# Optimization experiments

Hardware: AMD Instinct MI355X
Metric: run time of the kernel (lower is better)

## Reference

```python
import jax, jax.numpy as jnp
import numpy as np

N_NODES = 50000
N_EDGES = 400000
DIMS = [512, 512, 512, 512]  # input + 3 hidden
NUM_CLASSES = 40


def setup_inputs() -> dict:
    key = jax.random.key(0)
    ks = jax.random.split(key, 16)
    feat = jax.random.normal(ks[0], (N_NODES, DIMS[0]), dtype=jnp.float32)
    src = jax.random.randint(ks[1], (N_EDGES,), 0, N_NODES, dtype=jnp.int32)
    dst = jax.random.randint(ks[2], (N_EDGES,), 0, N_NODES, dtype=jnp.int32)
    params = {}
    for i in range(3):
        fan_in = DIMS[i]
        s = 1.0 / np.sqrt(fan_in)
        params[f"W{i}"] = jax.random.uniform(ks[3 + 2 * i], (DIMS[i], DIMS[i + 1]), jnp.float32, -s, s)
        params[f"b{i}"] = jax.random.uniform(ks[4 + 2 * i], (DIMS[i + 1],), jnp.float32, -s, s)
    s = 1.0 / np.sqrt(DIMS[-1])
    params["Wc"] = jax.random.uniform(ks[10], (DIMS[-1], NUM_CLASSES), jnp.float32, -s, s)
    params["bc"] = jax.random.uniform(ks[11], (NUM_CLASSES,), jnp.float32, -s, s)
    return {"feat": feat, "src": src, "dst": dst, **params}


def _gin_layer(h, src, dst, W, b):
    # DGL GINConv, aggregator='sum', eps=0: rst = (1+eps)*h + sum_{j in N(i)} h_j
    agg = jax.ops.segment_sum(h[src], dst, num_segments=N_NODES)  # [N, D]
    return jax.nn.relu((h + agg) @ W + b)  # apply_func Linear, then relu (dropout p=0)


def reference(feat, src, dst, W0, b0, W1, b1, W2, b2, Wc, bc):
    h = _gin_layer(feat, src, dst, W0, b0)
    h = _gin_layer(h, src, dst, W1, b1)
    h = _gin_layer(h, src, dst, W2, b2)
    return h @ Wc + bc  # [N, num_classes]
```

## Files before the change

kernel.cpp:

```cpp
#include <hip/hip_runtime.h>

#define N_NODES 50000
#define N_EDGES 400000
#define D 512
#define NCLS 40
#define SCAN_BLOCKS ((N_NODES + 255) / 256)

typedef __attribute__((ext_vector_type(8))) __bf16 bf16x8;
typedef __attribute__((ext_vector_type(4))) float f32x4;
typedef __attribute__((ext_vector_type(4))) float float4v;
typedef __attribute__((ext_vector_type(8))) unsigned short ushort8v;
typedef __attribute__((ext_vector_type(4))) unsigned short ushort4v;

__device__ __forceinline__ float bf2f(unsigned short u) {
  union { unsigned int i; float f; } v; v.i = ((unsigned int)u) << 16; return v.f;
}
__device__ __forceinline__ unsigned short f2bf(float f) {
  union { float f; unsigned int i; } v; v.f = f;
  unsigned int u = v.i;
  u += 0x7fffu + ((u >> 16) & 1u);
  return (unsigned short)(u >> 16);
}

__global__ void hist_kernel(const int* __restrict__ dst, int* __restrict__ counts) {
  int e = blockIdx.x * blockDim.x + threadIdx.x;
  if (e < N_EDGES) atomicAdd(&counts[dst[e]], 1);
}

__global__ __launch_bounds__(256) void scan_local_kernel(const int* __restrict__ counts,
    int* __restrict__ incl, int* __restrict__ bsum) {
  __shared__ int s[256];
  int i = blockIdx.x * 256 + threadIdx.x;
  int v = (i < N_NODES) ? counts[i] : 0;
  s[threadIdx.x] = v;
  __syncthreads();
#pragma unroll
  for (int o = 1; o < 256; o <<= 1) {
    int t = (threadIdx.x >= o) ? s[threadIdx.x - o] : 0;
    __syncthreads();
    s[threadIdx.x] += t;
    __syncthreads();
  }
  if (i < N_NODES) incl[i] = s[threadIdx.x];
  if (threadIdx.x == 255) bsum[blockIdx.x] = s[255];
}

__global__ __launch_bounds__(256) void scan_bsum_kernel(int* __restrict__ bsum) {
  __shared__ int s[256];
  int v = (threadIdx.x < SCAN_BLOCKS) ? bsum[threadIdx.x] : 0;
  s[threadIdx.x] = v;
  __syncthreads();
#pragma unroll
  for (int o = 1; o < 256; o <<= 1) {
    int t = (threadIdx.x >= o) ? s[threadIdx.x - o] : 0;
    __syncthreads();
    s[threadIdx.x] += t;
    __syncthreads();
  }
  if (threadIdx.x < SCAN_BLOCKS) bsum[threadIdx.x] = s[threadIdx.x] - v;
}

__global__ __launch_bounds__(256) void scan_finish_kernel(const int* __restrict__ counts,
    const int* __restrict__ bsum, int* __restrict__ row_ptr, int* __restrict__ cursor) {
  int i = blockIdx.x * 256 + threadIdx.x;
  if (i < N_NODES) {
    int inc = cursor[i] + bsum[blockIdx.x];
    row_ptr[i + 1] = inc;
    cursor[i] = inc - counts[i];
    if (i == 0) row_ptr[0] = 0;
  }
}

__global__ void fill_kernel(const int* __restrict__ src, const int* __restrict__ dst,
                            int* __restrict__ cursor, int* __restrict__ esrc) {
  int e = blockIdx.x * blockDim.x + threadIdx.x;
  if (e < N_EDGES) {
    int pos = atomicAdd(&cursor[dst[e]], 1);
    esrc[pos] = src[e];
  }
}

__global__ void cvt_feat_kernel(const float* __restrict__ feat, unsigned short* __restrict__ hb) {
  size_t i = (size_t)(blockIdx.x * blockDim.x + threadIdx.x) * 4;
  if (i < (size_t)N_NODES * D) {
    float4v v = *(const float4v*)&feat[i];
    ushort4v o;
    o[0] = f2bf(v[0]); o[1] = f2bf(v[1]); o[2] = f2bf(v[2]); o[3] = f2bf(v[3]);
    *(ushort4v*)&hb[i] = o;
  }
}

__global__ void cvt_w_kernel(const float* __restrict__ W, unsigned short* __restrict__ Wt) {
  int i = blockIdx.x * blockDim.x + threadIdx.x;
  int n = i >> 9, k = i & 511;
  Wt[i] = f2bf(W[k * D + n]);
}

__global__ void cvt_wc_kernel(const float* __restrict__ Wc, unsigned short* __restrict__ Wct) {
  int i = blockIdx.x * blockDim.x + threadIdx.x;
  if (i < 48 * D) {
    int n = i >> 9, k = i & 511;
    Wct[i] = (n < NCLS) ? f2bf(Wc[k * NCLS + n]) : (unsigned short)0;
  }
}

__global__ __launch_bounds__(256) void agg_kernel(const unsigned short* __restrict__ hb,
    const int* __restrict__ row_ptr, const int* __restrict__ esrc,
    unsigned short* __restrict__ zb) {
  int w = threadIdx.x >> 6, lane = threadIdx.x & 63;
  int node = blockIdx.x * 4 + w;
  int col = lane * 8;
  const unsigned short* hcol = hb + col;
  float acc[8];
  ushort8v v = *(const ushort8v*)&hcol[(size_t)node * D];
#pragma unroll
  for (int t = 0; t < 8; ++t) acc[t] = bf2f(v[t]);
  int s = row_ptr[node], e = row_ptr[node + 1];
  int j = s;
  for (; j + 4 <= e; j += 4) {
    int i0 = esrc[j + 0];
    int i1 = esrc[j + 1];
    int i2 = esrc[j + 2];
    int i3 = esrc[j + 3];
    ushort8v v0 = *(const ushort8v*)&hcol[(size_t)i0 * D];
    ushort8v v1 = *(const ushort8v*)&hcol[(size_t)i1 * D];
    ushort8v v2 = *(const ushort8v*)&hcol[(size_t)i2 * D];
    ushort8v v3 = *(const ushort8v*)&hcol[(size_t)i3 * D];
#pragma unroll
    for (int t = 0; t < 8; ++t) acc[t] += bf2f(v0[t]);
#pragma unroll
    for (int t = 0; t < 8; ++t) acc[t] += bf2f(v1[t]);
#pragma unroll
    for (int t = 0; t < 8; ++t) acc[t] += bf2f(v2[t]);
#pragma unroll
    for (int t = 0; t < 8; ++t) acc[t] += bf2f(v3[t]);
  }
  for (; j < e; ++j) {
    int sn = esrc[j];
    ushort8v nv = *(const ushort8v*)&hcol[(size_t)sn * D];
#pragma unroll
    for (int t = 0; t < 8; ++t) acc[t] += bf2f(nv[t]);
  }
  ushort8v o;
#pragma unroll
  for (int t = 0; t < 8; ++t) o[t] = f2bf(acc[t]);
  *(ushort8v*)&zb[(size_t)node * D + col] = o;
}

__global__ __launch_bounds__(256) void gemm_kernel(
    const unsigned short* __restrict__ Z, const unsigned short* __restrict__ Wt,
    const float* __restrict__ bias, unsigned short* __restrict__ Hout, int M) {
  __shared__ unsigned short smem[128 * 132];
  unsigned short* As = smem;
  unsigned short* Bs = smem + 4096;
  const int n0 = blockIdx.x * 128;
  const int m0 = blockIdx.y * 128;
  const int tid = threadIdx.x;
  const int lane = tid & 63;
  const int w = tid >> 6;
  const int wm = (w & 1) * 64;
  const int wn = (w >> 1) * 64;
  const int quad = lane >> 4;
  const int r16 = lane & 15;

  f32x4 acc[4][4];
#pragma unroll
  for (int i = 0; i < 4; ++i)
#pragma unroll
    for (int j = 0; j < 4; ++j)
      acc[i][j] = (f32x4){0.f, 0.f, 0.f, 0.f};

  const int c0 = w * 2;
  for (int kt = 0; kt < 16; ++kt) {
    __syncthreads();
    const int kbase = kt * 32;
#pragma unroll
    for (int c = 0; c < 2; ++c) {
      int chunk = c0 + c;
      int mrow = chunk * 16 + (lane >> 2);
      int kk = kbase + (lane & 3) * 8;
      int gm = m0 + mrow; if (gm > M - 1) gm = M - 1;
      __builtin_amdgcn_global_load_lds(
          (__attribute__((address_space(1))) void*)(void*)(Z + (size_t)gm * D + kk),
          (__attribute__((address_space(3))) void*)(As + chunk * 512),
          16, 0, 0);
      int nrow = n0 + mrow;
      __builtin_amdgcn_global_load_lds(
          (__attribute__((address_space(1))) void*)(void*)(Wt + (size_t)nrow * D + kk),
          (__attribute__((address_space(3))) void*)(Bs + chunk * 512),
          16, 0, 0);
    }
    __syncthreads();

    bf16x8 a[4], b[4];
#pragma unroll
    for (int i = 0; i < 4; ++i) {
      a[i] = *(const bf16x8*)&As[(wm + i * 16 + r16) * 32 + quad * 8];
      b[i] = *(const bf16x8*)&Bs[(wn + i * 16 + r16) * 32 + quad * 8];
    }
#pragma unroll
    for (int i = 0; i < 4; ++i)
#pragma unroll
      for (int j = 0; j < 4; ++j)
        acc[i][j] = __builtin_amdgcn_mfma_f32_16x16x32_bf16(a[i], b[j], acc[i][j], 0, 0, 0);
  }

  __syncthreads();
  unsigned short* Cs = smem;
#pragma unroll
  for (int j = 0; j < 4; ++j) {
    float bv = bias[n0 + wn + j * 16 + r16];
#pragma unroll
    for (int i = 0; i < 4; ++i) {
      int crow = wm + i * 16 + quad * 4;
      int ccol = wn + j * 16 + r16;
#pragma unroll
      for (int r = 0; r < 4; ++r) {
        float vv = acc[i][j][r] + bv;
        vv = vv > 0.f ? vv : 0.f;
        Cs[(crow + r) * 132 + ccol] = f2bf(vv);
      }
    }
  }
  __syncthreads();
#pragma unroll
  for (int it = 0; it < 8; ++it) {
    int row = w * 32 + it * 4 + (lane >> 4);
    int colofs = (lane & 15) * 8;
    int gm = m0 + row;
    if (gm < M) {
      ushort8v vv = *(const ushort8v*)&Cs[row * 132 + colofs];
      *(ushort8v*)&Hout[(size_t)gm * D + n0 + colofs] = vv;
    }
  }
}

__global__ __launch_bounds__(256) void cls_kernel(const unsigned short* __restrict__ hb,
    const unsigned short* __restrict__ Wct, const float* __restrict__ bc,
    float* __restrict__ out) {
  int w = threadIdx.x >> 6, lane = threadIdx.x & 63;
  int quad = lane >> 4, r16 = lane & 15;
  int nb = blockIdx.x * 64 + w * 16;
  int arow = nb + r16; if (arow > N_NODES - 1) arow = N_NODES - 1;
  f32x4 acc[3];
#pragma unroll
  for (int j = 0; j < 3; ++j) acc[j] = (f32x4){0.f, 0.f, 0.f, 0.f};
#pragma unroll 4
  for (int kt = 0; kt < 16; ++kt) {
    int kk = kt * 32 + quad * 8;
    bf16x8 a = *(const bf16x8*)&hb[(size_t)arow * D + kk];
#pragma unroll
    for (int j = 0; j < 3; ++j) {
      bf16x8 b = *(const bf16x8*)&Wct[(size_t)(j * 16 + r16) * D + kk];
      acc[j] = __builtin_amdgcn_mfma_f32_16x16x32_bf16(a, b, acc[j], 0, 0, 0);
    }
  }
#pragma unroll
  for (int j = 0; j < 3; ++j) {
    int gn = j * 16 + r16;
    if (gn < NCLS) {
      float bv = bc[gn];
#pragma unroll
      for (int r = 0; r < 4; ++r) {
        int gm = nb + quad * 4 + r;
        if (gm < N_NODES) out[(size_t)gm * NCLS + gn] = acc[j][r] + bv;
      }
    }
  }
}

extern "C" void kernel_launch(void* const* d_in, const int* in_sizes, int n_in,
                              void* d_out, int out_size, void* d_ws, size_t ws_size,
                              hipStream_t stream) {
  const float* feat = (const float*)d_in[0];
  const int* src = (const int*)d_in[1];
  const int* dst = (const int*)d_in[2];
  const float* W0 = (const float*)d_in[3];
  const float* b0 = (const float*)d_in[4];
  const float* W1 = (const float*)d_in[5];
  const float* b1 = (const float*)d_in[6];
  const float* W2 = (const float*)d_in[7];
  const float* b2 = (const float*)d_in[8];
  const float* Wc = (const float*)d_in[9];
  const float* bc = (const float*)d_in[10];
  float* out = (float*)d_out;

  char* ws = (char*)d_ws;
  size_t off = 0;
  auto alloc = [&](size_t bytes) {
    char* p = ws + off;
    off += (bytes + 255) & ~(size_t)255;
    return p;
  };
  unsigned short* hb = (unsigned short*)alloc((size_t)N_NODES * D * 2);
  unsigned short* zb = (unsigned short*)alloc((size_t)N_NODES * D * 2);
  unsigned short* Wt = (unsigned short*)alloc((size_t)3 * D * D * 2);
  unsigned short* Wct = (unsigned short*)alloc((size_t)48 * D * 2);
  int* row_ptr = (int*)alloc((size_t)(N_NODES + 1) * 4);
  int* counts  = (int*)alloc((size_t)N_NODES * 4);
  int* cursor  = (int*)alloc((size_t)N_NODES * 4);
  int* esrc    = (int*)alloc((size_t)N_EDGES * 4);
  int* bsum    = (int*)alloc((size_t)256 * 4);

  hipMemsetAsync(counts, 0, (size_t)N_NODES * 4, stream);
  hist_kernel<<<(N_EDGES + 255) / 256, 256, 0, stream>>>(dst, counts);
  scan_local_kernel<<<SCAN_BLOCKS, 256, 0, stream>>>(counts, cursor, bsum);
  scan_bsum_kernel<<<1, 256, 0, stream>>>(bsum);
  scan_finish_kernel<<<SCAN_BLOCKS, 256, 0, stream>>>(counts, bsum, row_ptr, cursor);
  fill_kernel<<<(N_EDGES + 255) / 256, 256, 0, stream>>>(src, dst, cursor, esrc);

  cvt_feat_kernel<<<(N_NODES * D / 4 + 255) / 256, 256, 0, stream>>>(feat, hb);
  cvt_w_kernel<<<1024, 256, 0, stream>>>(W0, Wt);
  cvt_w_kernel<<<1024, 256, 0, stream>>>(W1, Wt + (size_t)D * D);
  cvt_w_kernel<<<1024, 256, 0, stream>>>(W2, Wt + (size_t)2 * D * D);
  cvt_wc_kernel<<<(48 * D + 255) / 256, 256, 0, stream>>>(Wc, Wct);

  dim3 ggrid(4, (N_NODES + 127) / 128);
  const float* bs[3] = {b0, b1, b2};
  for (int l = 0; l < 3; ++l) {
    agg_kernel<<<N_NODES / 4, 256, 0, stream>>>(hb, row_ptr, esrc, zb);
    gemm_kernel<<<ggrid, 256, 0, stream>>>(zb, Wt + (size_t)l * D * D, bs[l], hb, N_NODES);
  }
  cls_kernel<<<(N_NODES + 63) / 64, 256, 0, stream>>>(hb, Wct, bc, out);
}
```

Before: 621.7 us.

## Fuse neighbor aggregation and GEMM into persistent tiled kernel with atomic work queue

Replaces the separate aggregation and GEMM kernels with one persistent kernel. Each block grabs a 32-node tile from an atomic counter, gathers the neighbor sums into LDS, and multiplies them against the weight matrix read directly from global memory with MFMA. Results go out through nontemporal stores into ping-pong buffers. This drops the round trip of the intermediate Z matrix through global memory and one launch per layer. The cost is that the whole weight matrix is re-read for every tile (relying on cache), M-tiles are small, and there is no double buffering of the gather against the MFMA work.

```diff
diff --git a/kernel.cpp b/kernel.cpp
--- a/kernel.cpp
+++ b/kernel.cpp
@@ -5,6 +5,8 @@
 #define D 512
 #define NCLS 40
 #define SCAN_BLOCKS ((N_NODES + 255) / 256)
+#define N_TILES ((N_NODES + 31) / 32)
+#define ZSTRIDE 520
 
 typedef __attribute__((ext_vector_type(8))) __bf16 bf16x8;
 typedef __attribute__((ext_vector_type(4))) float f32x4;
@@ -104,134 +106,113 @@
   }
 }
 
-__global__ __launch_bounds__(256) void agg_kernel(const unsigned short* __restrict__ hb,
-    const int* __restrict__ row_ptr, const int* __restrict__ esrc,
-    unsigned short* __restrict__ zb) {
-  int w = threadIdx.x >> 6, lane = threadIdx.x & 63;
-  int node = blockIdx.x * 4 + w;
-  int col = lane * 8;
-  const unsigned short* hcol = hb + col;
-  float acc[8];
-  ushort8v v = *(const ushort8v*)&hcol[(size_t)node * D];
-#pragma unroll
-  for (int t = 0; t < 8; ++t) acc[t] = bf2f(v[t]);
-  int s = row_ptr[node], e = row_ptr[node + 1];
-  int j = s;
-  for (; j + 4 <= e; j += 4) {
-    int i0 = esrc[j + 0];
-    int i1 = esrc[j + 1];
-    int i2 = esrc[j + 2];
-    int i3 = esrc[j + 3];
-    ushort8v v0 = *(const ushort8v*)&hcol[(size_t)i0 * D];
-    ushort8v v1 = *(const ushort8v*)&hcol[(size_t)i1 * D];
-    ushort8v v2 = *(const ushort8v*)&hcol[(size_t)i2 * D];
-    ushort8v v3 = *(const ushort8v*)&hcol[(size_t)i3 * D];
-#pragma unroll
-    for (int t = 0; t < 8; ++t) acc[t] += bf2f(v0[t]);
-#pragma unroll
-    for (int t = 0; t < 8; ++t) acc[t] += bf2f(v1[t]);
-#pragma unroll
-    for (int t = 0; t < 8; ++t) acc[t] += bf2f(v2[t]);
-#pragma unroll
-    for (int t = 0; t < 8; ++t) acc[t] += bf2f(v3[t]);
-  }
-  for (; j < e; ++j) {
-    int sn = esrc[j];
-    ushort8v nv = *(const ushort8v*)&hcol[(size_t)sn * D];
-#pragma unroll
-    for (int t = 0; t < 8; ++t) acc[t] += bf2f(nv[t]);
-  }
-  ushort8v o;
-#pragma unroll
-  for (int t = 0; t < 8; ++t) o[t] = f2bf(acc[t]);
-  *(ushort8v*)&zb[(size_t)node * D + col] = o;
-}
-
-__global__ __launch_bounds__(256) void gemm_kernel(
-    const unsigned short* __restrict__ Z, const unsigned short* __restrict__ Wt,
-    const float* __restrict__ bias, unsigned short* __restrict__ Hout, int M) {
-  __shared__ unsigned short smem[128 * 132];
-  unsigned short* As = smem;
-  unsigned short* Bs = smem + 4096;
-  const int n0 = blockIdx.x * 128;
-  const int m0 = blockIdx.y * 128;
+__global__ __launch_bounds__(256, 4) void fused_kernel(
+    const unsigned short* __restrict__ Hin, const int* __restrict__ row_ptr,
+    const int* __restrict__ esrc, const unsigned short* __restrict__ Wt,
+    const float* __restrict__ bias, unsigned short* __restrict__ Hout,
+    int* __restrict__ counter) {
+  __shared__ unsigned short Zs[32 * ZSTRIDE];
+  __shared__ int tile_s;
   const int tid = threadIdx.x;
   const int lane = tid & 63;
   const int w = tid >> 6;
-  const int wm = (w & 1) * 64;
-  const int wn = (w >> 1) * 64;
-  const int quad = lane >> 4;
-  const int r16 = lane & 15;
-
-  f32x4 acc[4][4];
-#pragma unroll
-  for (int i = 0; i < 4; ++i)
-#pragma unroll
-    for (int j = 0; j < 4; ++j)
-      acc[i][j] = (f32x4){0.f, 0.f, 0.f, 0.f};
-
-  const int c0 = w * 2;
-  for (int kt = 0; kt < 16; ++kt) {
-    __syncthreads();
-    const int kbase = kt * 32;
-#pragma unroll
-    for (int c = 0; c < 2; ++c) {
-      int chunk = c0 + c;
-      int mrow = chunk * 16 + (lane >> 2);
-      int kk = kbase + (lane & 3) * 8;
-      int gm = m0 + mrow; if (gm > M - 1) gm = M - 1;
-      __builtin_amdgcn_global_load_lds(
-          (__attribute__((address_space(1))) void*)(void*)(Z + (size_t)gm * D + kk),
-          (__attribute__((address_space(3))) void*)(As + chunk * 512),
-          16, 0, 0);
-      int nrow = n0 + mrow;
-      __builtin_amdgcn_global_load_lds(
-          (__attribute__((address_space(1))) void*)(void*)(Wt + (size_t)nrow * D + kk),
-          (__attribute__((address_space(3))) void*)(Bs + chunk * 512),
-          16, 0, 0);
-    }
-    __syncthreads();
-
-    bf16x8 a[4], b[4];
-#pragma unroll
-    for (int i = 0; i < 4; ++i) {
-      a[i] = *(const bf16x8*)&As[(wm + i * 16 + r16) * 32 + quad * 8];
-      b[i] = *(const bf16x8*)&Bs[(wn + i * 16 + r16) * 32 + quad * 8];
-    }
-#pragma unroll
-    for (int i = 0; i < 4; ++i)
-#pragma unroll
-      for (int j = 0; j < 4; ++j)
-        acc[i][j] = __builtin_amdgcn_mfma_f32_16x16x32_bf16(a[i], b[j], acc[i][j], 0, 0, 0);
-  }
-
-  __syncthreads();
-  unsigned short* Cs = smem;
-#pragma unroll
-  for (int j = 0; j < 4; ++j) {
-    float bv = bias[n0 + wn + j * 16 + r16];
-#pragma unroll
-    for (int i = 0; i < 4; ++i) {
-      int crow = wm + i * 16 + quad * 4;
-      int ccol = wn + j * 16 + r16;
-#pragma unroll
-      for (int r = 0; r < 4; ++r) {
-        float vv = acc[i][j][r] + bv;
-        vv = vv > 0.f ? vv : 0.f;
-        Cs[(crow + r) * 132 + ccol] = f2bf(vv);
-      }
-    }
-  }
-  __syncthreads();
-#pragma unroll
-  for (int it = 0; it < 8; ++it) {
-    int row = w * 32 + it * 4 + (lane >> 4);
-    int colofs = (lane & 15) * 8;
-    int gm = m0 + row;
-    if (gm < M) {
-      ushort8v vv = *(const ushort8v*)&Cs[row * 132 + colofs];
-      *(ushort8v*)&Hout[(size_t)gm * D + n0 + colofs] = vv;
-    }
+  const int quad = lane >> 4, r16 = lane & 15;
+  const int col = lane * 8;
+
+  for (;;) {
+    if (tid == 0) tile_s = atomicAdd(counter, 1);
+    __syncthreads();
+    const int tile = tile_s;
+    if (tile >= N_TILES) break;
+    const int m0 = tile * 32;
+
+    for (int i = 0; i < 8; ++i) {
+      int nl = w * 8 + i;
+      int node = m0 + nl;
+      float acc[8];
+      if (node < N_NODES) {
+        ushort8v v = *(const ushort8v*)&Hin[(size_t)node * D + col];
+#pragma unroll
+        for (int t = 0; t < 8; ++t) acc[t] = bf2f(v[t]);
+        int s = row_ptr[node], e = row_ptr[node + 1];
+        int j = s;
+        for (; j + 4 <= e; j += 4) {
+          int i0 = esrc[j + 0], i1 = esrc[j + 1], i2 = esrc[j + 2], i3 = esrc[j + 3];
+          ushort8v v0 = *(const ushort8v*)&Hin[(size_t)i0 * D + col];
+          ushort8v v1 = *(const ushort8v*)&Hin[(size_t)i1 * D + col];
+          ushort8v v2 = *(const ushort8v*)&Hin[(size_t)i2 * D + col];
+          ushort8v v3 = *(const ushort8v*)&Hin[(size_t)i3 * D + col];
+#pragma unroll
+          for (int t = 0; t < 8; ++t) acc[t] += bf2f(v0[t]);
+#pragma unroll
+          for (int t = 0; t < 8; ++t) acc[t] += bf2f(v1[t]);
+#pragma unroll
+          for (int t = 0; t < 8; ++t) acc[t] += bf2f(v2[t]);
+#pragma unroll
+          for (int t = 0; t < 8; ++t) acc[t] += bf2f(v3[t]);
+        }
+        for (; j < e; ++j) {
+          int sn = esrc[j];
+          ushort8v nv = *(const ushort8v*)&Hin[(size_t)sn * D + col];
+#pragma unroll
+          for (int t = 0; t < 8; ++t) acc[t] += bf2f(nv[t]);
+        }
+      } else {
+#pragma unroll
+        for (int t = 0; t < 8; ++t) acc[t] = 0.f;
+      }
+      ushort8v o;
+#pragma unroll
+      for (int t = 0; t < 8; ++t) o[t] = f2bf(acc[t]);
+      *(ushort8v*)&Zs[nl * ZSTRIDE + col] = o;
+    }
+    __syncthreads();
+
+    const int wn = w * 128;
+    f32x4 c[2][8];
+#pragma unroll
+    for (int i = 0; i < 2; ++i)
+#pragma unroll
+      for (int j = 0; j < 8; ++j) c[i][j] = (f32x4){0.f, 0.f, 0.f, 0.f};
+#pragma unroll
+    for (int kt = 0; kt < 16; ++kt) {
+      int kk = kt * 32 + quad * 8;
+      bf16x8 a0 = *(const bf16x8*)&Zs[r16 * ZSTRIDE + kk];
+      bf16x8 a1 = *(const bf16x8*)&Zs[(16 + r16) * ZSTRIDE + kk];
+#pragma unroll
+      for (int j = 0; j < 8; ++j) {
+        bf16x8 b = *(const bf16x8*)&Wt[(size_t)(wn + j * 16 + r16) * D + kk];
+        c[0][j] = __builtin_amdgcn_mfma_f32_16x16x32_bf16(a0, b, c[0][j], 0, 0, 0);
+        c[1][j] = __builtin_amdgcn_mfma_f32_16x16x32_bf16(a1, b, c[1][j], 0, 0, 0);
+      }
+    }
+    __syncthreads();
+
+#pragma unroll
+    for (int j = 0; j < 8; ++j) {
+      float bv = bias[wn + j * 16 + r16];
+#pragma unroll
+      for (int i = 0; i < 2; ++i) {
+        int crow = i * 16 + quad * 4;
+#pragma unroll
+        for (int r = 0; r < 4; ++r) {
+          float vv = c[i][j][r] + bv;
+          vv = vv > 0.f ? vv : 0.f;
+          Zs[(crow + r) * ZSTRIDE + wn + j * 16 + r16] = f2bf(vv);
+        }
+      }
+    }
+    __syncthreads();
+#pragma unroll
+    for (int i = 0; i < 8; ++i) {
+      int row = w * 8 + i;
+      int gm = m0 + row;
+      if (gm < N_NODES) {
+        ushort8v vv = *(const ushort8v*)&Zs[row * ZSTRIDE + col];
+        __builtin_nontemporal_store(vv, (ushort8v*)&Hout[(size_t)gm * D + col]);
+      }
+    }
+    __syncthreads();
   }
 }
 
@@ -301,8 +282,10 @@
   int* cursor  = (int*)alloc((size_t)N_NODES * 4);
   int* esrc    = (int*)alloc((size_t)N_EDGES * 4);
   int* bsum    = (int*)alloc((size_t)256 * 4);
+  int* ctrs    = (int*)alloc((size_t)4 * 4);
 
   hipMemsetAsync(counts, 0, (size_t)N_NODES * 4, stream);
+  hipMemsetAsync(ctrs, 0, 16, stream);
   hist_kernel<<<(N_EDGES + 255) / 256, 256, 0, stream>>>(dst, counts);
   scan_local_kernel<<<SCAN_BLOCKS, 256, 0, stream>>>(counts, cursor, bsum);
   scan_bsum_kernel<<<1, 256, 0, stream>>>(bsum);
@@ -315,11 +298,11 @@
   cvt_w_kernel<<<1024, 256, 0, stream>>>(W2, Wt + (size_t)2 * D * D);
   cvt_wc_kernel<<<(48 * D + 255) / 256, 256, 0, stream>>>(Wc, Wct);
 
-  dim3 ggrid(4, (N_NODES + 127) / 128);
   const float* bs[3] = {b0, b1, b2};
+  unsigned short* bufs[2] = {hb, zb};
   for (int l = 0; l < 3; ++l) {
-    agg_kernel<<<N_NODES / 4, 256, 0, stream>>>(hb, row_ptr, esrc, zb);
-    gemm_kernel<<<ggrid, 256, 0, stream>>>(zb, Wt + (size_t)l * D * D, bs[l], hb, N_NODES);
-  }
-  cls_kernel<<<(N_NODES + 63) / 64, 256, 0, stream>>>(hb, Wct, bc, out);
-}
+    fused_kernel<<<1024, 256, 0, stream>>>(bufs[l & 1], row_ptr, esrc,
+        Wt + (size_t)l * D * D, bs[l], bufs[(l + 1) & 1], ctrs + l);
+  }
+  cls_kernel<<<(N_NODES + 63) / 64, 256, 0, stream>>>(zb, Wct, bc, out);
+}
```

After: 1.218 ms. 1.96x slower.

## Double GEMM K-tile to 64 with XOR-swizzled LDS layout; merge weight conversions

Applied to the files above, without the earlier changes.

The GEMM now stages 64-wide K tiles, so it runs 8 iterations instead of 16 and halves the barrier pairs. Each 16-byte chunk is placed in LDS with an XOR swizzle on the row index, which is meant to avoid bank conflicts when the MFMA fragments are read. The three per-layer weight transpose/convert launches are merged into one launch. Shared memory still fits inside the existing 128x132 buffer, and the output epilogue reuses that same region.

```diff
diff --git a/kernel.cpp b/kernel.cpp
--- a/kernel.cpp
+++ b/kernel.cpp
@@ -11,6 +11,9 @@
 typedef __attribute__((ext_vector_type(4))) float float4v;
 typedef __attribute__((ext_vector_type(8))) unsigned short ushort8v;
 typedef __attribute__((ext_vector_type(4))) unsigned short ushort4v;
+
+#define AS1 __attribute__((address_space(1)))
+#define AS3 __attribute__((address_space(3)))
 
 __device__ __forceinline__ float bf2f(unsigned short u) {
   union { unsigned int i; float f; } v; v.i = ((unsigned int)u) << 16; return v.f;
@@ -90,9 +93,13 @@
   }
 }
 
-__global__ void cvt_w_kernel(const float* __restrict__ W, unsigned short* __restrict__ Wt) {
+__global__ void cvt_w3_kernel(const float* __restrict__ W0, const float* __restrict__ W1,
+                              const float* __restrict__ W2, unsigned short* __restrict__ Wt) {
   int i = blockIdx.x * blockDim.x + threadIdx.x;
-  int n = i >> 9, k = i & 511;
+  int l = i >> 18;
+  int r = i & 262143;
+  int n = r >> 9, k = r & 511;
+  const float* W = (l == 0) ? W0 : ((l == 1) ? W1 : W2);
   Wt[i] = f2bf(W[k * D + n]);
 }
 
@@ -118,10 +125,7 @@
   int s = row_ptr[node], e = row_ptr[node + 1];
   int j = s;
   for (; j + 4 <= e; j += 4) {
-    int i0 = esrc[j + 0];
-    int i1 = esrc[j + 1];
-    int i2 = esrc[j + 2];
-    int i3 = esrc[j + 3];
+    int i0 = esrc[j + 0], i1 = esrc[j + 1], i2 = esrc[j + 2], i3 = esrc[j + 3];
     ushort8v v0 = *(const ushort8v*)&hcol[(size_t)i0 * D];
     ushort8v v1 = *(const ushort8v*)&hcol[(size_t)i1 * D];
     ushort8v v2 = *(const ushort8v*)&hcol[(size_t)i2 * D];
@@ -152,7 +156,7 @@
     const float* __restrict__ bias, unsigned short* __restrict__ Hout, int M) {
   __shared__ unsigned short smem[128 * 132];
   unsigned short* As = smem;
-  unsigned short* Bs = smem + 4096;
+  unsigned short* Bs = smem + 8192;
   const int n0 = blockIdx.x * 128;
   const int m0 = blockIdx.y * 128;
   const int tid = threadIdx.x;
@@ -162,6 +166,8 @@
   const int wn = (w >> 1) * 64;
   const int quad = lane >> 4;
   const int r16 = lane & 15;
+  const int srow = lane >> 3;
+  const int sslot = lane & 7;
 
   f32x4 acc[4][4];
 #pragma unroll
@@ -170,39 +176,41 @@
     for (int j = 0; j < 4; ++j)
       acc[i][j] = (f32x4){0.f, 0.f, 0.f, 0.f};
 
-  const int c0 = w * 2;
-  for (int kt = 0; kt < 16; ++kt) {
-    __syncthreads();
-    const int kbase = kt * 32;
-#pragma unroll
-    for (int c = 0; c < 2; ++c) {
-      int chunk = c0 + c;
-      int mrow = chunk * 16 + (lane >> 2);
-      int kk = kbase + (lane & 3) * 8;
-      int gm = m0 + mrow; if (gm > M - 1) gm = M - 1;
+  for (int kt = 0; kt < 8; ++kt) {
+    __syncthreads();
+    const int kbase = kt * 64;
+#pragma unroll
+    for (int c = 0; c < 4; ++c) {
+      int r0 = w * 32 + c * 8;
+      int row = r0 + srow;
+      int gk = kbase + (sslot ^ (row & 7)) * 8;
+      int gm = m0 + row; if (gm > M - 1) gm = M - 1;
       __builtin_amdgcn_global_load_lds(
-          (__attribute__((address_space(1))) void*)(void*)(Z + (size_t)gm * D + kk),
-          (__attribute__((address_space(3))) void*)(As + chunk * 512),
-          16, 0, 0);
-      int nrow = n0 + mrow;
+          (AS1 void*)(void*)(Z + (size_t)gm * D + gk),
+          (AS3 void*)(As + r0 * 64), 16, 0, 0);
+      int gn = n0 + row;
       __builtin_amdgcn_global_load_lds(
-          (__attribute__((address_space(1))) void*)(void*)(Wt + (size_t)nrow * D + kk),
-          (__attribute__((address_space(3))) void*)(Bs + chunk * 512),
-          16, 0, 0);
-    }
-    __syncthreads();
-
-    bf16x8 a[4], b[4];
-#pragma unroll
-    for (int i = 0; i < 4; ++i) {
-      a[i] = *(const bf16x8*)&As[(wm + i * 16 + r16) * 32 + quad * 8];
-      b[i] = *(const bf16x8*)&Bs[(wn + i * 16 + r16) * 32 + quad * 8];
-    }
-#pragma unroll
-    for (int i = 0; i < 4; ++i)
-#pragma unroll
-      for (int j = 0; j < 4; ++j)
-        acc[i][j] = __builtin_amdgcn_mfma_f32_16x16x32_bf16(a[i], b[j], acc[i][j], 0, 0, 0);
+          (AS1 void*)(void*)(Wt + (size_t)gn * D + gk),
+          (AS3 void*)(Bs + r0 * 64), 16, 0, 0);
+    }
+    __syncthreads();
+
+#pragma unroll
+    for (int half = 0; half < 2; ++half) {
+      bf16x8 a[4], b[4];
+#pragma unroll
+      for (int i = 0; i < 4; ++i) {
+        int ra = wm + i * 16 + r16;
+        a[i] = *(const bf16x8*)&As[ra * 64 + (((half << 2) + quad) ^ (ra & 7)) * 8];
+        int rb = wn + i * 16 + r16;
+        b[i] = *(const bf16x8*)&Bs[rb * 64 + (((half << 2) + quad) ^ (rb & 7)) * 8];
+      }
+#pragma unroll
+      for (int i = 0; i < 4; ++i)
+#pragma unroll
+        for (int j = 0; j < 4; ++j)
+          acc[i][j] = __builtin_amdgcn_mfma_f32_16x16x32_bf16(a[i], b[j], acc[i][j], 0, 0, 0);
+    }
   }
 
   __syncthreads();
@@ -310,9 +318,7 @@
   fill_kernel<<<(N_EDGES + 255) / 256, 256, 0, stream>>>(src, dst, cursor, esrc);
 
   cvt_feat_kernel<<<(N_NODES * D / 4 + 255) / 256, 256, 0, stream>>>(feat, hb);
-  cvt_w_kernel<<<1024, 256, 0, stream>>>(W0, Wt);
-  cvt_w_kernel<<<1024, 256, 0, stream>>>(W1, Wt + (size_t)D * D);
-  cvt_w_kernel<<<1024, 256, 0, stream>>>(W2, Wt + (size_t)2 * D * D);
+  cvt_w3_kernel<<<3 * 262144 / 256, 256, 0, stream>>>(W0, W1, W2, Wt);
   cvt_wc_kernel<<<(48 * D + 255) / 256, 256, 0, stream>>>(Wc, Wct);
 
   dim3 ggrid(4, (N_NODES + 127) / 128);
```

Measured after the change: 627.6 us. No clear change (+1.0%).
